# Kernel optimization log

Measured on AMD Instinct MI355X. Metric: run time of the kernel, lower is better.

The kernel has to match this reference:

```python
import jax, jax.numpy as jnp
import numpy as np

B, T, C = 4, 2048, 1024
H = 16
HS = C // H  # 64
FF = 4 * C  # 4096


def setup_inputs() -> dict:
    key = jax.random.key(0)
    ks = jax.random.split(key, 10)
    s_in = C ** -0.5
    s_ff = FF ** -0.5
    return {
        "x": jax.random.normal(ks[0], (B, T, C), dtype=jnp.float32),
        "Wq": jax.random.normal(ks[1], (H, C, HS), dtype=jnp.float32) * s_in,
        "Wk": jax.random.normal(ks[2], (H, C, HS), dtype=jnp.float32) * s_in,
        "Wv": jax.random.normal(ks[3], (H, C, HS), dtype=jnp.float32) * s_in,
        "Wproj": jax.random.normal(ks[4], (C, C), dtype=jnp.float32) * s_in,
        "bproj": jax.random.normal(ks[5], (C,), dtype=jnp.float32) * 0.01,
        "W1": jax.random.normal(ks[6], (C, FF), dtype=jnp.float32) * s_in,
        "b1": jax.random.normal(ks[7], (FF,), dtype=jnp.float32) * 0.01,
        "W2": jax.random.normal(ks[8], (FF, C), dtype=jnp.float32) * s_ff,
        "b2": jax.random.normal(ks[9], (C,), dtype=jnp.float32) * 0.01,
    }


def reference(x, Wq, Wk, Wv, Wproj, bproj, W1, b1, W2, b2):
    b, t, c = x.shape
    # per-head projections, batched over heads: [B,H,T,HS]
    q = jnp.einsum("btc,hcd->bhtd", x, Wq)
    k = jnp.einsum("btc,hcd->bhtd", x, Wk)
    v = jnp.einsum("btc,hcd->bhtd", x, Wv)
    # NOTE: original scales by full embed dim c**-0.5, not head_size
    scores = jnp.einsum("bhtd,bhsd->bhts", q, k) * (c ** -0.5)
    causal = jnp.tril(jnp.ones((t, t), dtype=bool))
    scores = jnp.where(causal[None, None], scores, -jnp.inf)
    w = jax.nn.softmax(scores, axis=-1)
    y = jnp.einsum("bhts,bhsd->bhtd", w, v)  # [B,H,T,HS]
    y = jnp.transpose(y, (0, 2, 1, 3)).reshape(b, t, c)  # concat heads
    attn_out = y @ Wproj + bproj
    x = attn_out + x
    ff = jax.nn.relu(x @ W1 + b1) @ W2 + b2
    return ff + x
```

## Files before the change

### kernel.cpp

```cpp
#include <hip/hip_runtime.h>

typedef unsigned short u16;
typedef __attribute__((ext_vector_type(4))) float f32x4;
typedef __attribute__((ext_vector_type(8))) short bf16x8;

constexpr int kB  = 4;
constexpr int kT  = 2048;
constexpr int kC  = 1024;
constexpr int kH  = 16;
constexpr int kFF = 4096;
constexpr int kM  = kB * kT;
constexpr int k3C = 3 * kC;

__device__ __forceinline__ float b2f(u16 u) {
    union { unsigned int i; float f; } v;
    v.i = ((unsigned int)u) << 16;
    return v.f;
}
__device__ __forceinline__ u16 f2b(float f) {
    union { float f; unsigned int i; } v;
    v.f = f;
    unsigned int r = (v.i + 0x7FFFu + ((v.i >> 16) & 1u)) >> 16;
    return (u16)r;
}

__device__ __forceinline__ void lds_barrier() {
    __asm__ __volatile__("" ::: "memory");
    __builtin_amdgcn_s_waitcnt(0xC07F);
    __builtin_amdgcn_s_barrier();
    __asm__ __volatile__("" ::: "memory");
}

__global__ void cvt_f32_bf16(const float* __restrict__ in, u16* __restrict__ out, int n4)
{
    const int i = blockIdx.x * 256 + threadIdx.x;
    if (i >= n4) return;
    float4 v = *(const float4*)(in + (size_t)i * 4);
    ushort4 o;
    o.x = f2b(v.x); o.y = f2b(v.y); o.z = f2b(v.z); o.w = f2b(v.w);
    *(ushort4*)(out + (size_t)i * 4) = o;
}

__global__ void transpose_cvt(const float* __restrict__ in, int R, int Cc,
                              u16* __restrict__ out)
{
    __shared__ float t[32][33];
    const int bx = blockIdx.x * 32;
    const int by = blockIdx.y * 32;
    const int lx = threadIdx.x, ly = threadIdx.y;
    #pragma unroll
    for (int i = 0; i < 32; i += 8)
        t[ly + i][lx] = in[(size_t)(by + ly + i) * Cc + bx + lx];
    __syncthreads();
    #pragma unroll
    for (int i = 0; i < 32; i += 8)
        out[(size_t)(bx + ly + i) * R + by + lx] = f2b(t[lx][ly + i]);
}

__global__ void repack_qkv_t(const float* __restrict__ Wq, const float* __restrict__ Wk,
                             const float* __restrict__ Wv, u16* __restrict__ out)
{
    __shared__ float t[32][33];
    const int z = blockIdx.z;
    const int s = z >> 4, h = z & 15;
    const float* in = (s == 0 ? Wq : s == 1 ? Wk : Wv) + (size_t)h * (kC * 64);
    const int bx = blockIdx.x * 32;
    const int by = blockIdx.y * 32;
    const int lx = threadIdx.x, ly = threadIdx.y;
    #pragma unroll
    for (int i = 0; i < 32; i += 8)
        t[ly + i][lx] = in[(size_t)(by + ly + i) * 64 + bx + lx];
    __syncthreads();
    const int orow = s * kC + h * 64 + bx;
    #pragma unroll
    for (int i = 0; i < 32; i += 8)
        out[(size_t)(orow + ly + i) * kC + by + lx] = f2b(t[lx][ly + i]);
}

__global__ __launch_bounds__(512, 4) void gemm_bt_k32r(
    const u16* __restrict__ A, int lda,
    const u16* __restrict__ Bt, int ldb,
    int K,
    const float* __restrict__ bias,
    const u16* __restrict__ resid,
    float* __restrict__ CoF,
    u16* __restrict__ CoB,
    int ldc, int do_relu, int nbx)
{
    __shared__ __align__(16) u16 As[3][256 * 32];
    __shared__ __align__(16) u16 Bs[3][128 * 32];

    const int tid  = threadIdx.x;
    const int wave = tid >> 6, lane = tid & 63;
    const int wm = (wave >> 1) * 64, wn = (wave & 1) * 64;

    const int cpx = gridDim.x >> 3;
    const int swz = (blockIdx.x & 7) * cpx + (blockIdx.x >> 3);
    const int bx = swz % nbx, by = swz / nbx;
    const int m0 = by * 256, n0 = bx * 128;

    const int rl = tid >> 2;
    const int cg = ((tid & 3) ^ ((tid >> 3) & 3)) * 8;

    const int fm = lane & 15, fkq = lane >> 4;
    const int fchunk = (fkq ^ ((fm >> 1) & 3)) * 8;

    f32x4 acc[4][4];
    #pragma unroll
    for (int i = 0; i < 4; ++i)
        #pragma unroll
        for (int j = 0; j < 4; ++j)
            acc[i][j] = (f32x4){0.f, 0.f, 0.f, 0.f};

    const int NT = K >> 5;

    auto stg = [&](const u16* g, int ld, int r0, u16* l) {
        __builtin_amdgcn_global_load_lds(
            (const __attribute__((address_space(1))) void*)(g + (size_t)(r0 + rl) * ld + cg),
            (__attribute__((address_space(3))) void*)(l + r0 * 32 + tid * 8), 16, 0, 0);
    };
    auto stageAB = [&](int kt, int slot) {
        const u16* ga = A  + (size_t)m0 * lda + kt * 32;
        const u16* gb = Bt + (size_t)n0 * ldb + kt * 32;
        stg(ga, lda, 0,   As[slot]);
        stg(ga, lda, 128, As[slot]);
        stg(gb, ldb, 0,   Bs[slot]);
    };

    stageAB(0, 0);
    if (NT > 1) {
        stageAB(1, 1);
        __builtin_amdgcn_sched_barrier(0);
        __asm__ __volatile__("s_waitcnt vmcnt(3)" ::: "memory");
    } else {
        __builtin_amdgcn_sched_barrier(0);
        __asm__ __volatile__("s_waitcnt vmcnt(0)" ::: "memory");
    }
    __builtin_amdgcn_s_barrier();
    __builtin_amdgcn_sched_barrier(0);

    int cur = 0;
    for (int t = 0; t < NT; ++t) {
        const int sst = (cur == 0) ? 2 : cur - 1;
        if (t + 2 < NT) stageAB(t + 2, sst);
        const u16* Sa = As[cur];
        const u16* Sb = Bs[cur];
        bf16x8 a[4], b[4];
        #pragma unroll
        for (int i = 0; i < 4; ++i) {
            const int m = wm + i * 16 + fm;
            a[i] = *(const bf16x8*)&Sa[m * 32 + fchunk];
        }
        #pragma unroll
        for (int j = 0; j < 4; ++j) {
            const int n = wn + j * 16 + fm;
            b[j] = *(const bf16x8*)&Sb[n * 32 + fchunk];
        }
        __builtin_amdgcn_s_setprio(1);
        #pragma unroll
        for (int i = 0; i < 4; ++i)
            #pragma unroll
            for (int j = 0; j < 4; ++j)
                acc[i][j] = __builtin_amdgcn_mfma_f32_16x16x32_bf16(
                    a[i], b[j], acc[i][j], 0, 0, 0);
        __builtin_amdgcn_s_setprio(0);
        if (t + 1 < NT) {
            __builtin_amdgcn_sched_barrier(0);
            if (t + 2 < NT) { __asm__ __volatile__("s_waitcnt vmcnt(3)" ::: "memory"); }
            else            { __asm__ __volatile__("s_waitcnt vmcnt(0)" ::: "memory"); }
            __builtin_amdgcn_s_barrier();
            __builtin_amdgcn_sched_barrier(0);
        }
        cur = (cur == 2) ? 0 : cur + 1;
    }

    const int col = lane & 15;
    const int rb  = (lane >> 4) * 4;
    #pragma unroll
    for (int i = 0; i < 4; ++i) {
        #pragma unroll
        for (int j = 0; j < 4; ++j) {
            const int n = n0 + wn + j * 16 + col;
            #pragma unroll
            for (int r = 0; r < 4; ++r) {
                const int m = m0 + wm + i * 16 + rb + r;
                float v = acc[i][j][r];
                if (bias)    v += bias[n];
                if (do_relu) v = fmaxf(v, 0.f);
                if (resid)   v += b2f(resid[(size_t)m * ldc + n]);
                if (CoF) CoF[(size_t)m * ldc + n] = v;
                else     CoB[(size_t)m * ldc + n] = f2b(v);
            }
        }
    }
}

__global__ __launch_bounds__(256) void attn_mfma3(
    const u16* __restrict__ QKV, u16* __restrict__ Y)
{
    __shared__ __align__(16) u16 Kl[2][64 * 64];
    __shared__ __align__(16) u16 Vt[2][64 * 64];
    __shared__ __align__(16) u16 Pl[4][16 * 64];

    const int tid  = threadIdx.x;
    const int wave = tid >> 6, lane = tid & 63;
    const int ln = lane & 15, quad = lane >> 4;
    const int idx = blockIdx.x;
    const int bh = idx & 63;
    const int qt = 15 - (idx >> 6);
    const int b = bh >> 4, h = bh & 15;
    const int q0 = qt << 7;
    const int bT = b * kT;
    const int qgw = q0 + wave * 32;
    const float scale = 0.03125f;

    const u16* kvbase = QKV + (size_t)bT * k3C + kC + h * 64;

    const int sK = tid >> 3, cK = tid & 7;
    const int sV = (tid >> 3) * 2, cV = tid & 7;
    const int kwa0 = (sK << 6) + ((cK ^ (sK & 7)) << 3);
    const int kwa1 = kwa0 + (32 << 6);

    bf16x8 qa[2][2];
    #pragma unroll
    for (int qsub = 0; qsub < 2; ++qsub) {
        const size_t qb = ((size_t)bT + qgw + 16 * qsub + ln) * k3C + h * 64;
        qa[qsub][0] = *(const bf16x8*)(QKV + qb + quad * 8);
        qa[qsub][1] = *(const bf16x8*)(QKV + qb + 32 + quad * 8);
    }

    f32x4 acco[2][4];
    #pragma unroll
    for (int qsub = 0; qsub < 2; ++qsub)
        #pragma unroll
        for (int jd = 0; jd < 4; ++jd) acco[qsub][jd] = (f32x4){0.f, 0.f, 0.f, 0.f};
    float mrun[2] = {-1e30f, -1e30f}, lrun[2] = {0.f, 0.f};
    u16* Pw = Pl[wave];

    const int ntiles = 2 * qt + 2;

    auto loadkv = [&](int s0p, uint4& k0, uint4& k1, uint4& v0, uint4& v1) {
        const u16* kg = kvbase + (size_t)(s0p + sK) * k3C + cK * 8;
        k0 = *(const uint4*)kg;
        k1 = *(const uint4*)(kg + (size_t)32 * k3C);
        const u16* vg = kvbase + kC + (size_t)(s0p + sV) * k3C + cV * 8;
        v0 = *(const uint4*)vg;
        v1 = *(const uint4*)(vg + k3C);
    };
    auto stage = [&](u16* Kb, u16* Vb, const uint4& k0, const uint4& k1,
                     const uint4& v0, const uint4& v1) {
        *(uint4*)&Kb[kwa0] = k0;
        *(uint4*)&Kb[kwa1] = k1;
        const u16* t0 = (const u16*)&v0;
        const u16* t1 = (const u16*)&v1;
        #pragma unroll
        for (int i = 0; i < 8; ++i) {
            const int d = cV * 8 + i;
            const int chunk = ((sV >> 3) ^ (d & 7) ^ ((d >> 3) & 7)) & 7;
            ushort2 pr; pr.x = t0[i]; pr.y = t1[i];
            *(ushort2*)&Vb[(d << 6) + (chunk << 3) + (sV & 7)] = pr;
        }
    };
    auto compute = [&](int t, const u16* Kb, const u16* Vb) {
        const int s0 = t << 6;
        if (s0 > qgw + 31) return;
        f32x4 accs[2][4];
        #pragma unroll
        for (int qsub = 0; qsub < 2; ++qsub)
            #pragma unroll
            for (int j = 0; j < 4; ++j) accs[qsub][j] = (f32x4){0.f, 0.f, 0.f, 0.f};
        __builtin_amdgcn_s_setprio(1);
        #pragma unroll
        for (int ks = 0; ks < 2; ++ks) {
            #pragma unroll
            for (int j = 0; j < 4; ++j) {
                const int s = j * 16 + ln;
                bf16x8 kb = *(const bf16x8*)&Kb[(s << 6) + ((((quad + 4 * ks) ^ (s & 7)) & 7) << 3)];
                accs[0][j] = __builtin_amdgcn_mfma_f32_16x16x32_bf16(kb, qa[0][ks], accs[0][j], 0, 0, 0);
                accs[1][j] = __builtin_amdgcn_mfma_f32_16x16x32_bf16(kb, qa[1][ks], accs[1][j], 0, 0, 0);
            }
        }
        __builtin_amdgcn_s_setprio(0);
        bf16x8 vfr[4][2];
        #pragma unroll
        for (int jd = 0; jd < 4; ++jd) {
            const int d = jd * 16 + ln;
            #pragma unroll
            for (int ks = 0; ks < 2; ++ks)
                vfr[jd][ks] = *(const bf16x8*)&Vb[(d << 6) + ((((quad + 4 * ks) ^ (d & 7) ^ ((d >> 3) & 7)) & 7) << 3)];
        }
        #pragma unroll
        for (int qsub = 0; qsub < 2; ++qsub) {
            const int qg = qgw + 16 * qsub + ln;
            float part = -1e30f;
            #pragma unroll
            for (int j = 0; j < 4; ++j) {
                #pragma unroll
                for (int r = 0; r < 4; ++r) {
                    const int sg = s0 + j * 16 + quad * 4 + r;
                    float v = accs[qsub][j][r] * scale;
                    v = (sg <= qg) ? v : -1e30f;
                    accs[qsub][j][r] = v;
                    part = fmaxf(part, v);
                }
            }
            float mx = fmaxf(part, __shfl_xor(part, 16));
            mx = fmaxf(mx, __shfl_xor(mx, 32));
            const bool skip = __all(mx - mrun[qsub] <= 8.0f);
            const float mn = skip ? mrun[qsub] : fmaxf(mrun[qsub], mx);
            float ls = 0.f;
            #pragma unroll
            for (int j = 0; j < 4; ++j)
                #pragma unroll
                for (int r = 0; r < 4; ++r) {
                    const float p = __expf(accs[qsub][j][r] - mn);
                    accs[qsub][j][r] = p;
                    ls += p;
                }
            ls += __shfl_xor(ls, 16);
            ls += __shfl_xor(ls, 32);
            if (skip) {
                lrun[qsub] += ls;
            } else {
                const float al = __expf(mrun[qsub] - mn);
                mrun[qsub] = mn;
                lrun[qsub] = lrun[qsub] * al + ls;
                #pragma unroll
                for (int jd = 0; jd < 4; ++jd)
                    #pragma unroll
                    for (int r = 0; r < 4; ++r)
                        acco[qsub][jd][r] *= al;
            }
            #pragma unroll
            for (int j = 0; j < 4; ++j) {
                ushort4 pk;
                pk.x = f2b(accs[qsub][j][0]); pk.y = f2b(accs[qsub][j][1]);
                pk.z = f2b(accs[qsub][j][2]); pk.w = f2b(accs[qsub][j][3]);
                const int chunk = ((2 * j + (quad >> 1)) ^ (ln & 7)) & 7;
                *(ushort4*)&Pw[(ln << 6) + (chunk << 3) + ((quad & 1) << 2)] = pk;
            }
            __builtin_amdgcn_s_setprio(1);
            #pragma unroll
            for (int ks = 0; ks < 2; ++ks) {
                bf16x8 pb = *(const bf16x8*)&Pw[(ln << 6) + ((((4 * ks + quad) ^ (ln & 7)) & 7) << 3)];
                #pragma unroll
                for (int jd = 0; jd < 4; ++jd)
                    acco[qsub][jd] = __builtin_amdgcn_mfma_f32_16x16x32_bf16(
                        vfr[jd][ks], pb, acco[qsub][jd], 0, 0, 0);
            }
            __builtin_amdgcn_s_setprio(0);
        }
    };

    uint4 ka0, ka1, va0, va1, kb0, kb1, vb0, vb1;
    loadkv(0, ka0, ka1, va0, va1);
    for (int t = 0; t < ntiles; t += 2) {
        stage(Kl[0], Vt[0], ka0, ka1, va0, va1);
        loadkv((t + 1) << 6, kb0, kb1, vb0, vb1);
        lds_barrier();
        compute(t, Kl[0], Vt[0]);
        stage(Kl[1], Vt[1], kb0, kb1, vb0, vb1);
        loadkv(((t + 2) < ntiles ? (t + 2) : 0) << 6, ka0, ka1, va0, va1);
        lds_barrier();
        compute(t + 1, Kl[1], Vt[1]);
    }

    #pragma unroll
    for (int qsub = 0; qsub < 2; ++qsub) {
        const float inv = 1.f / lrun[qsub];
        const size_t yrow = ((size_t)bT + qgw + 16 * qsub + ln) * kC + h * 64;
        #pragma unroll
        for (int jd = 0; jd < 4; ++jd) {
            ushort4 ov;
            ov.x = f2b(acco[qsub][jd][0] * inv);
            ov.y = f2b(acco[qsub][jd][1] * inv);
            ov.z = f2b(acco[qsub][jd][2] * inv);
            ov.w = f2b(acco[qsub][jd][3] * inv);
            *(ushort4*)(Y + yrow + jd * 16 + quad * 4) = ov;
        }
    }
}

extern "C" void kernel_launch(void* const* d_in, const int* in_sizes, int n_in,
                              void* d_out, int out_size, void* d_ws, size_t ws_size,
                              hipStream_t stream) {
    const float* x     = (const float*)d_in[0];
    const float* Wq    = (const float*)d_in[1];
    const float* Wk    = (const float*)d_in[2];
    const float* Wv    = (const float*)d_in[3];
    const float* Wproj = (const float*)d_in[4];
    const float* bproj = (const float*)d_in[5];
    const float* W1    = (const float*)d_in[6];
    const float* b1    = (const float*)d_in[7];
    const float* W2    = (const float*)d_in[8];
    const float* b2    = (const float*)d_in[9];

    u16* ws      = (u16*)d_ws;
    u16* QKV     = ws;
    u16* ffh     = ws;
    u16* attn_y  = ws + (size_t)kM * kFF;
    u16* xb      = attn_y  + (size_t)kM * kC;
    u16* res1    = xb      + (size_t)kM * kC;
    u16* Wqkv_t  = res1    + (size_t)kM * kC;
    u16* Wproj_t = Wqkv_t  + (size_t)k3C * kC;
    u16* W1t     = Wproj_t + (size_t)kC * kC;
    u16* W2t     = W1t     + (size_t)kFF * kC;
    float* out   = (float*)d_out;

    cvt_f32_bf16<<<(kM * kC / 4 + 255) / 256, 256, 0, stream>>>(x, xb, kM * kC / 4);
    repack_qkv_t<<<dim3(2, kC / 32, 48), dim3(32, 8), 0, stream>>>(Wq, Wk, Wv, Wqkv_t);
    transpose_cvt<<<dim3(kC / 32, kC / 32),  dim3(32, 8), 0, stream>>>(Wproj, kC, kC, Wproj_t);
    transpose_cvt<<<dim3(kFF / 32, kC / 32), dim3(32, 8), 0, stream>>>(W1, kC, kFF, W1t);
    transpose_cvt<<<dim3(kC / 32, kFF / 32), dim3(32, 8), 0, stream>>>(W2, kFF, kC, W2t);

    gemm_bt_k32r<<<dim3((kM / 256) * (k3C / 128)), 512, 0, stream>>>(
        xb, kC, Wqkv_t, kC, kC, nullptr, nullptr, nullptr, QKV, k3C, 0, k3C / 128);
    attn_mfma3<<<dim3(1024), 256, 0, stream>>>(QKV, attn_y);
    gemm_bt_k32r<<<dim3((kM / 256) * (kC / 128)), 512, 0, stream>>>(
        attn_y, kC, Wproj_t, kC, kC, bproj, xb, nullptr, res1, kC, 0, kC / 128);
    gemm_bt_k32r<<<dim3((kM / 256) * (kFF / 128)), 512, 0, stream>>>(
        res1, kC, W1t, kC, kC, b1, nullptr, nullptr, ffh, kFF, 1, kFF / 128);
    gemm_bt_k32r<<<dim3((kM / 256) * (kC / 128)), 512, 0, stream>>>(
        ffh, kFF, W2t, kFF, kFF, b2, res1, out, nullptr, kC, 0, kC / 128);
}
```

Measured before the change: 561.0 us.

## Add 256x256-tile eight-phase pipelined GEMM for the FFN up-projection

Adds a new bf16 GEMM kernel with 256x256 output tiles, K-step 64, and double-buffered A/B halves loaded directly into LDS. The loop is split into eight phases in which LDS reads, async global loads and MFMA blocks are interleaved, pinned with scheduler barriers and explicit waitcnts. It also raises MFMA priority and swizzles the block order. Only the W1 GEMM (with bias and ReLU) uses it, aiming for more data reuse per tile and better overlap of loads with compute. The cost is higher register pressure, lower occupancy (2 blocks per CU) and a fragile hand-written schedule.

Result: slower. 575.7 us (+2.6%).

```diff
diff --git a/kernel.cpp b/kernel.cpp
--- a/kernel.cpp
+++ b/kernel.cpp
@@ -29,6 +29,16 @@
     __builtin_amdgcn_s_waitcnt(0xC07F);
     __builtin_amdgcn_s_barrier();
     __asm__ __volatile__("" ::: "memory");
+}
+
+__device__ __forceinline__ void bar_pinned() {
+    __builtin_amdgcn_sched_barrier(0);
+    __builtin_amdgcn_s_barrier();
+    __builtin_amdgcn_sched_barrier(0);
+}
+__device__ __forceinline__ void lgkm0_pinned() {
+    __asm__ __volatile__("s_waitcnt lgkmcnt(0)" ::: "memory");
+    __builtin_amdgcn_sched_barrier(0);
 }
 
 __global__ void cvt_f32_bf16(const float* __restrict__ in, u16* __restrict__ out, int n4)
@@ -75,6 +85,186 @@
     #pragma unroll
     for (int i = 0; i < 32; i += 8)
         out[(size_t)(orow + ly + i) * kC + by + lx] = f2b(t[lx][ly + i]);
+}
+
+__global__ __launch_bounds__(512, 2) void gemm_bt_8ph(
+    const u16* __restrict__ A, int lda,
+    const u16* __restrict__ Bt, int ldb,
+    int K,
+    const float* __restrict__ bias,
+    const u16* __restrict__ resid,
+    float* __restrict__ CoF,
+    u16* __restrict__ CoB,
+    int ldc, int do_relu, int nbx)
+{
+    __shared__ __align__(16) u16 As[2][2][128 * 64];
+    __shared__ __align__(16) u16 Bs[2][2][128 * 64];
+
+    const int tid  = threadIdx.x;
+    const int wave = tid >> 6, lane = tid & 63;
+    const int wm = wave >> 2, wn = wave & 3;
+
+    const int cpx = gridDim.x >> 3;
+    const int swz = (blockIdx.x & 7) * cpx + (blockIdx.x >> 3);
+    const int bx = swz % nbx, by = swz / nbx;
+    const int m0 = by * 256, n0 = bx * 256;
+
+    const int srow = tid >> 3, sc = tid & 7;
+    const int fm = lane & 15, fkq = lane >> 4;
+
+    f32x4 acc[8][4];
+    #pragma unroll
+    for (int i = 0; i < 8; ++i)
+        #pragma unroll
+        for (int j = 0; j < 4; ++j)
+            acc[i][j] = (f32x4){0.f, 0.f, 0.f, 0.f};
+
+    const int NT = K >> 6;
+    const int NI = NT >> 1;
+
+    auto stageHalf = [&](const u16* g, int ld, u16* lh) {
+        {
+            const int row = srow;
+            const int cg  = (sc ^ (row & 7)) * 8;
+            __builtin_amdgcn_global_load_lds(
+                (const __attribute__((address_space(1))) void*)(g + (size_t)row * ld + cg),
+                (__attribute__((address_space(3))) void*)(lh + tid * 8), 16, 0, 0);
+        }
+        {
+            const int row = 64 + srow;
+            const int cg  = (sc ^ (row & 7)) * 8;
+            __builtin_amdgcn_global_load_lds(
+                (const __attribute__((address_space(1))) void*)(g + (size_t)row * ld + cg),
+                (__attribute__((address_space(3))) void*)(lh + 4096 + tid * 8), 16, 0, 0);
+        }
+    };
+    auto stA = [&](int kt, int ha) {
+        stageHalf(A + (size_t)(m0 + ha * 128) * lda + kt * 64, lda, As[kt & 1][ha]);
+    };
+    auto stB = [&](int kt, int hb) {
+        stageHalf(Bt + (size_t)(n0 + hb * 128) * ldb + kt * 64, ldb, Bs[kt & 1][hb]);
+    };
+
+    auto rdA = [&](bf16x8 (&a)[4][2], int db, int qm) {
+        #pragma unroll
+        for (int i = 0; i < 4; ++i) {
+            const int ra = qm * 64 + i * 16 + fm;
+            #pragma unroll
+            for (int ks = 0; ks < 2; ++ks) {
+                const int slot = (ks * 4 + fkq) ^ (ra & 7);
+                a[i][ks] = *(const bf16x8*)&As[db][wm][ra * 64 + slot * 8];
+            }
+        }
+    };
+    auto rdB = [&](bf16x8 (&b)[2][2], int db, int qn) {
+        #pragma unroll
+        for (int j = 0; j < 2; ++j) {
+            const int rb = (wn & 1) * 64 + qn * 32 + j * 16 + fm;
+            #pragma unroll
+            for (int ks = 0; ks < 2; ++ks) {
+                const int slot = (ks * 4 + fkq) ^ (rb & 7);
+                b[j][ks] = *(const bf16x8*)&Bs[db][wn >> 1][rb * 64 + slot * 8];
+            }
+        }
+    };
+    auto mm = [&](bf16x8 (&a)[4][2], bf16x8 (&b)[2][2], int qm, int qn) {
+        __builtin_amdgcn_s_setprio(1);
+        #pragma unroll
+        for (int ks = 0; ks < 2; ++ks)
+            #pragma unroll
+            for (int i = 0; i < 4; ++i)
+                #pragma unroll
+                for (int j = 0; j < 2; ++j)
+                    acc[qm * 4 + i][qn * 2 + j] = __builtin_amdgcn_mfma_f32_16x16x32_bf16(
+                        a[i][ks], b[j][ks], acc[qm * 4 + i][qn * 2 + j], 0, 0, 0);
+        __builtin_amdgcn_s_setprio(0);
+    };
+
+    stA(0, 0); stA(0, 1); stB(0, 0); stB(0, 1);
+    if (NT > 1) {
+        stB(1, 0); stB(1, 1);
+        __builtin_amdgcn_sched_barrier(0);
+        __asm__ __volatile__("s_waitcnt vmcnt(4)" ::: "memory");
+    } else {
+        __builtin_amdgcn_sched_barrier(0);
+        __asm__ __volatile__("s_waitcnt vmcnt(0)" ::: "memory");
+    }
+    bar_pinned();
+
+    bf16x8 aL[4][2], aH[4][2], bL[2][2], bH[2][2];
+    for (int it = 0; it < NI; ++it) {
+        const int t0 = 2 * it;
+        rdA(aL, 0, 0); rdB(bL, 0, 0);
+        stA(t0 + 1, 0);
+        bar_pinned(); lgkm0_pinned();
+        mm(aL, bL, 0, 0);
+        bar_pinned();
+        rdB(bH, 0, 1);
+        stA(t0 + 1, 1);
+        bar_pinned(); lgkm0_pinned();
+        mm(aL, bH, 0, 1);
+        bar_pinned();
+        rdA(aH, 0, 1);
+        if (t0 + 2 < NT) stB(t0 + 2, 0);
+        bar_pinned(); lgkm0_pinned();
+        mm(aH, bH, 1, 1);
+        bar_pinned();
+        if (t0 + 2 < NT) {
+            stB(t0 + 2, 1);
+            __builtin_amdgcn_sched_barrier(0);
+            __asm__ __volatile__("s_waitcnt vmcnt(4)" ::: "memory");
+        } else {
+            __builtin_amdgcn_sched_barrier(0);
+            __asm__ __volatile__("s_waitcnt vmcnt(0)" ::: "memory");
+        }
+        bar_pinned();
+        mm(aH, bL, 1, 0);
+        bar_pinned();
+        rdA(aL, 1, 0); rdB(bL, 1, 0);
+        if (t0 + 2 < NT) stA(t0 + 2, 0);
+        bar_pinned(); lgkm0_pinned();
+        mm(aL, bL, 0, 0);
+        bar_pinned();
+        rdB(bH, 1, 1);
+        if (t0 + 2 < NT) stA(t0 + 2, 1);
+        bar_pinned(); lgkm0_pinned();
+        mm(aL, bH, 0, 1);
+        bar_pinned();
+        rdA(aH, 1, 1);
+        if (t0 + 3 < NT) stB(t0 + 3, 0);
+        bar_pinned(); lgkm0_pinned();
+        mm(aH, bH, 1, 1);
+        bar_pinned();
+        if (t0 + 3 < NT) stB(t0 + 3, 1);
+        if (it + 1 < NI) {
+            __builtin_amdgcn_sched_barrier(0);
+            __asm__ __volatile__("s_waitcnt vmcnt(4)" ::: "memory");
+        }
+        bar_pinned();
+        mm(aH, bL, 1, 0);
+        bar_pinned();
+    }
+
+    const int col = lane & 15;
+    const int rb4 = (lane >> 4) * 4;
+    #pragma unroll
+    for (int i8 = 0; i8 < 8; ++i8) {
+        const int mb = m0 + wm * 128 + (i8 >> 2) * 64 + (i8 & 3) * 16 + rb4;
+        #pragma unroll
+        for (int j4 = 0; j4 < 4; ++j4) {
+            const int n = n0 + wn * 64 + (j4 >> 1) * 32 + (j4 & 1) * 16 + col;
+            #pragma unroll
+            for (int r = 0; r < 4; ++r) {
+                const int m = mb + r;
+                float v = acc[i8][j4][r];
+                if (bias)    v += bias[n];
+                if (do_relu) v = fmaxf(v, 0.f);
+                if (resid)   v += b2f(resid[(size_t)m * ldc + n]);
+                if (CoF) CoF[(size_t)m * ldc + n] = v;
+                else     CoB[(size_t)m * ldc + n] = f2b(v);
+            }
+        }
+    }
 }
 
 __global__ __launch_bounds__(512, 4) void gemm_bt_k32r(
@@ -418,8 +608,8 @@
     attn_mfma3<<<dim3(1024), 256, 0, stream>>>(QKV, attn_y);
     gemm_bt_k32r<<<dim3((kM / 256) * (kC / 128)), 512, 0, stream>>>(
         attn_y, kC, Wproj_t, kC, kC, bproj, xb, nullptr, res1, kC, 0, kC / 128);
-    gemm_bt_k32r<<<dim3((kM / 256) * (kFF / 128)), 512, 0, stream>>>(
-        res1, kC, W1t, kC, kC, b1, nullptr, nullptr, ffh, kFF, 1, kFF / 128);
+    gemm_bt_8ph<<<dim3((kM / 256) * (kFF / 256)), 512, 0, stream>>>(
+        res1, kC, W1t, kC, kC, b1, nullptr, nullptr, ffh, kFF, 1, kFF / 256);
     gemm_bt_k32r<<<dim3((kM / 256) * (kC / 128)), 512, 0, stream>>>(
         ffh, kFF, W2t, kFF, kFF, b2, res1, out, nullptr, kC, 0, kC / 128);
 }
```
